# Optimization experiments

Hardware: AMD Instinct MI355X
Metric: run time of the kernel (lower is better)

Reference implementation:

```python
import jax, jax.numpy as jnp
import numpy as np

B, T, D = 64, 512, 1024  # batch, step_dim, feature_dim


def setup_inputs() -> dict:
    key = jax.random.key(0)
    k1, k2, k3, k4, k5 = jax.random.split(key, 5)
    x = jax.random.normal(k1, (B, T, D), dtype=jnp.float32)
    mask = jax.random.randint(k2, (B, T), 0, 2).astype(bool)
    mask = mask.at[:, 0].set(True)  # guarantee >=1 valid token per row
    # xavier_uniform bounds
    w_bound = float(np.sqrt(6.0 / (D + D)))
    c_bound = float(np.sqrt(6.0 / (T + 1)))
    weight = jax.random.uniform(k3, (D, D), minval=-w_bound, maxval=w_bound, dtype=jnp.float32)
    context_vector = jax.random.uniform(k4, (T, 1), minval=-c_bound, maxval=c_bound, dtype=jnp.float32)
    b = jnp.zeros((T,), dtype=jnp.float32)
    return {"x": x, "mask": mask, "weight": weight, "context_vector": context_vector, "b": b}


def reference(x, mask, weight, context_vector, b):
    # batched bilinear scores: eij[b,t,s] = x[b,t,:] @ W @ x[b,s,:]^T
    xw = jnp.einsum('btd,de->bte', x, weight)          # [B,T,D]
    eij = jnp.einsum('bte,bse->bts', xw, x)            # [B,T,T]
    # bias over last axis (matches view(-1, T) + b), tanh
    eij = jnp.tanh(eij + b)                            # [B,T,T]
    # context-vector reduction over last axis -> [B,T]
    scores = jnp.einsum('bts,s->bt', eij, context_vector[:, 0])
    # masked softmax over T
    scores = jnp.where(mask, scores, -jnp.inf)
    a = jax.nn.softmax(scores, axis=1)                 # [B,T]
    # weighted sum of inputs -> [B,D]
    out = jnp.einsum('btd,bt->bd', x, a)
    return (out, a)
```

## Files before the change

kernel.cpp:

```cpp
#include <hip/hip_runtime.h>
#include <hip/hip_bf16.h>
#include <math.h>

#define B_ 64
#define T_ 512
#define D_ 1024
#define M_ (B_*T_)

typedef unsigned short u16;
typedef __attribute__((ext_vector_type(8))) _Float16 f16x8;
typedef __attribute__((ext_vector_type(4))) float f32x4;

__device__ __forceinline__ u16 f2h(float f) {
  union { _Float16 h; u16 u; } v;
  v.h = (_Float16)f;
  return v.u;
}

__device__ __forceinline__ float h2f(u16 u) {
  union { u16 u; _Float16 h; } v;
  v.u = u;
  return (float)v.h;
}

__device__ __forceinline__ float fast_tanh(float x) {
  return 1.0f - 2.0f / (__expf(2.0f * x) + 1.0f);
}

__device__ __forceinline__ void gll16(const void* g, void* l) {
  __builtin_amdgcn_global_load_lds(
      (const __attribute__((address_space(1))) unsigned int*)g,
      (__attribute__((address_space(3))) unsigned int*)l, 16, 0, 0);
}

__global__ __launch_bounds__(256) void cvt_x_kernel(const float4* __restrict__ x,
                                                    ushort4* __restrict__ xh, int n4) {
  int i = blockIdx.x * 256 + threadIdx.x;
  if (i < n4) {
    float4 v = x[i];
    ushort4 o;
    o.x = f2h(v.x); o.y = f2h(v.y); o.z = f2h(v.z); o.w = f2h(v.w);
    xh[i] = o;
  }
}

__global__ __launch_bounds__(1024) void cvt_wt_kernel(const float* __restrict__ W,
                                                      u16* __restrict__ Wt) {
  __shared__ float tile[32][33];
  int tx = threadIdx.x & 31, ty = threadIdx.x >> 5;
  int n0 = blockIdx.x * 32, k0 = blockIdx.y * 32;
  tile[ty][tx] = W[(k0 + ty) * D_ + n0 + tx];
  __syncthreads();
  Wt[(n0 + ty) * D_ + k0 + tx] = f2h(tile[tx][ty]);
}


__device__ __forceinline__ void gemm_core128(const u16* __restrict__ Abase,
                                             const u16* __restrict__ Bbase, int K,
                                             u16* As, u16* Bs, int tid, f32x4 acc[4][4]) {
  const int wave = tid >> 6, lane = tid & 63;
  const int swz_c = ((lane & 3) - ((lane >> 3) & 3)) & 3;
  const int rin = lane >> 2;
  const u16* gA[2]; u16* lA[2];
  const u16* gB[2]; u16* lB[2];
#pragma unroll
  for (int j = 0; j < 2; j++) {
    int ci = wave * 2 + j;
    gA[j] = Abase + (long)(ci * 16 + rin) * K + swz_c * 8;
    lA[j] = As + ci * 512;
    gB[j] = Bbase + (long)(ci * 16 + rin) * K + swz_c * 8;
    lB[j] = Bs + ci * 512;
  }
  const int wrow = (wave >> 1) * 64, wcol = (wave & 1) * 64;
  const int lm = lane & 15, qd = lane >> 4;
  const int swz_r = ((qd + (lm >> 1)) & 3) * 8;
  const u16* ra = As + (wrow + lm) * 32 + swz_r;
  const u16* rb = Bs + (wcol + lm) * 32 + swz_r;

  for (int kt = 0; kt < K; kt += 32) {
#pragma unroll
    for (int j = 0; j < 2; j++) {
      gll16(gA[j], lA[j]); gA[j] += 32;
      gll16(gB[j], lB[j]); gB[j] += 32;
    }
    __syncthreads();
    f16x8 af[4], bfr[4];
#pragma unroll
    for (int i = 0; i < 4; i++) {
      af[i] = *(const f16x8*)(ra + i * 512);
      bfr[i] = *(const f16x8*)(rb + i * 512);
    }
#pragma unroll
    for (int mi = 0; mi < 4; mi++)
#pragma unroll
      for (int ni = 0; ni < 4; ni++)
        acc[mi][ni] = __builtin_amdgcn_mfma_f32_16x16x32_f16(af[mi], bfr[ni], acc[mi][ni], 0, 0, 0);
    __syncthreads();
  }
}

__global__ __launch_bounds__(256, 4) void gemm1_kernel(const u16* __restrict__ xh,
                                                       const u16* __restrict__ wt,
                                                       u16* __restrict__ xw) {
  __shared__ u16 As[128 * 32], Bs[128 * 32];
  f32x4 acc[4][4] = {};
  const int tid = threadIdx.x;
  const int bx = blockIdx.x;
  const int xcd = bx & 7, j = bx >> 3;
  const int mt = xcd * 32 + (j >> 3);
  const int nt = j & 7;
  const long m0 = (long)mt * 128;
  const long n0 = (long)nt * 128;
  gemm_core128(xh + m0 * D_, wt + n0 * D_, D_, As, Bs, tid, acc);

  const int wave = tid >> 6, lane = tid & 63;
  const int wrow = (wave >> 1) * 64, wcol = (wave & 1) * 64;
  const int lm = lane & 15, qd = lane >> 4;
#pragma unroll
  for (int mi = 0; mi < 4; mi++)
#pragma unroll
    for (int ni = 0; ni < 4; ni++) {
      long m = m0 + wrow + mi * 16 + qd * 4;
      long n = n0 + wcol + ni * 16 + lm;
      u16* p = xw + m * D_ + n;
#pragma unroll
      for (int r = 0; r < 4; r++) p[(long)r * D_] = f2h(acc[mi][ni][r]);
    }
}

__global__ __launch_bounds__(256, 4) void gemm2_kernel(const u16* __restrict__ xw,
                                                       const u16* __restrict__ xh,
                                                       const float* __restrict__ bias,
                                                       const float* __restrict__ cv,
                                                       float* __restrict__ scores_part) {
  __shared__ u16 As[128 * 32], Bs[128 * 32];
  f32x4 acc[4][4] = {};
  const int bx = blockIdx.x;
  const int xcd = bx & 7, j = bx >> 3;
  const int bb = xcd * 8 + (j >> 4);
  const int tile = j & 15;
  const int tt = tile >> 2, st = tile & 3;
  const int tid = threadIdx.x;
  const long arow = (long)bb * T_ + tt * 128;
  const long brow = (long)bb * T_ + st * 128;
  gemm_core128(xw + arow * D_, xh + brow * D_, D_, As, Bs, tid, acc);

  const int wave = tid >> 6, lane = tid & 63;
  const int wrow = (wave >> 1) * 64, wcol = (wave & 1) * 64;
  const int lm = lane & 15, qd = lane >> 4;
  float cvv[4], bv[4];
#pragma unroll
  for (int ni = 0; ni < 4; ni++) {
    int s = st * 128 + wcol + ni * 16 + lm;
    cvv[ni] = cv[s];
    bv[ni] = bias[s];
  }
  const int plane = st * 2 + (wave & 1);
  float* dst = scores_part + plane * (B_ * T_) + bb * T_ + tt * 128;
#pragma unroll
  for (int mi = 0; mi < 4; mi++) {
#pragma unroll
    for (int r = 0; r < 4; r++) {
      float p = 0.f;
#pragma unroll
      for (int ni = 0; ni < 4; ni++) p += fast_tanh(acc[mi][ni][r] + bv[ni]) * cvv[ni];
      p += __shfl_xor(p, 1); p += __shfl_xor(p, 2);
      p += __shfl_xor(p, 4); p += __shfl_xor(p, 8);
      if (lm == 0) dst[wrow + mi * 16 + qd * 4 + r] = p;
    }
  }
}

__global__ __launch_bounds__(512) void softmax_kernel(const float* __restrict__ sp,
                                                      const unsigned char* __restrict__ m8,
                                                      float* __restrict__ a_out) {
  const int b = blockIdx.x, t = threadIdx.x;
  __shared__ int nonz;
  __shared__ float redm[8], reds[8];
  if (t == 0) nonz = 0;
  __syncthreads();
  unsigned char c = m8[t * 4 + 1] | m8[t * 4 + 2] | m8[t * 4 + 3];
  if (c) atomicOr(&nonz, 1);
  __syncthreads();
  const bool is_i32 = (nonz == 0);
  const int idx = b * T_ + t;
  const bool valid = is_i32 ? (m8[(long)idx * 4] != 0) : (m8[idx] != 0);

  float val = 0.f;
#pragma unroll
  for (int pl = 0; pl < 8; pl++) val += sp[pl * (B_ * T_) + idx];
  if (!valid) val = -INFINITY;
  float m = val;
#pragma unroll
  for (int o = 32; o > 0; o >>= 1) m = fmaxf(m, __shfl_xor(m, o));
  const int wv = t >> 6, ln = t & 63;
  if (ln == 0) redm[wv] = m;
  __syncthreads();
  float rowmax = redm[0];
#pragma unroll
  for (int i = 1; i < 8; i++) rowmax = fmaxf(rowmax, redm[i]);

  float e = valid ? expf(val - rowmax) : 0.f;
  float ssum = e;
#pragma unroll
  for (int o = 32; o > 0; o >>= 1) ssum += __shfl_xor(ssum, o);
  if (ln == 0) reds[wv] = ssum;
  __syncthreads();
  float tot = 0.f;
#pragma unroll
  for (int i = 0; i < 8; i++) tot += reds[i];
  a_out[idx] = e / tot;
}

__global__ __launch_bounds__(256) void wsum_kernel(const u16* __restrict__ xh,
                                                   const float* __restrict__ a,
                                                   float* __restrict__ out) {
  __shared__ float4 lred[4][64];
  const int b = blockIdx.x, dq = blockIdx.y, tid = threadIdx.x;
  const int w = tid >> 6, lane = tid & 63;
  const int d0 = dq * 256 + lane * 4;
  const u16* xp = xh + (long)b * T_ * D_ + d0;
  const float* ap = a + b * T_;
  float4 acc = make_float4(0.f, 0.f, 0.f, 0.f);
  for (int i = 0; i < 128; i++) {
    int t = w * 128 + i;
    float av = ap[t];
    ushort4 xv = *(const ushort4*)(xp + (long)t * D_);
    acc.x += av * h2f(xv.x); acc.y += av * h2f(xv.y);
    acc.z += av * h2f(xv.z); acc.w += av * h2f(xv.w);
  }
  lred[w][lane] = acc;
  __syncthreads();
  if (w == 0) {
    float4 s0 = lred[0][lane], s1 = lred[1][lane], s2 = lred[2][lane], s3 = lred[3][lane];
    float4 s;
    s.x = s0.x + s1.x + s2.x + s3.x;
    s.y = s0.y + s1.y + s2.y + s3.y;
    s.z = s0.z + s1.z + s2.z + s3.z;
    s.w = s0.w + s1.w + s2.w + s3.w;
    *(float4*)(out + (long)b * D_ + d0) = s;
  }
}

extern "C" void kernel_launch(void* const* d_in, const int* in_sizes, int n_in,
                              void* d_out, int out_size, void* d_ws, size_t ws_size,
                              hipStream_t stream) {
  const float* x = (const float*)d_in[0];
  const unsigned char* mask = (const unsigned char*)d_in[1];
  const float* W = (const float*)d_in[2];
  const float* cv = (const float*)d_in[3];
  const float* bias = (const float*)d_in[4];

  float* out = (float*)d_out;
  float* a_out = out + (size_t)B_ * D_;

  char* ws = (char*)d_ws;
  u16* xh = (u16*)(ws);
  u16* wt = (u16*)(ws + 67108864);
  float* scores_part = (float*)(ws + 67108864);
  u16* xw = (u16*)(ws + 69206016);

  cvt_x_kernel<<<(M_ * D_ / 4 + 255) / 256, 256, 0, stream>>>((const float4*)x,
                                                              (ushort4*)xh, M_ * D_ / 4);
  cvt_wt_kernel<<<dim3(32, 32), 1024, 0, stream>>>(W, wt);
  gemm1_kernel<<<2048, 256, 0, stream>>>(xh, wt, xw);
  gemm2_kernel<<<1024, 256, 0, stream>>>(xw, xh, bias, cv, scores_part);
  softmax_kernel<<<B_, 512, 0, stream>>>(scores_part, mask, a_out);
  wsum_kernel<<<dim3(B_, 4), 256, 0, stream>>>(xh, a_out, out);
}
```

Baseline: 344.4 us.

## Enlarge gemm1 tiles, merge conversion kernels, fuse softmax with weighted sum

gemm1 becomes a standalone kernel with a 256x128 output tile and a K-step of 64. It uses a new XOR-style LDS swizzle and drops to 2 blocks per CU, aiming for more data reuse per load and fewer barriers. The x and W conversion kernels are merged into a single launch, and the softmax and weighted-sum kernels are fused. Each fused block recomputes the softmax for its batch row, removing a launch and a global round-trip for the attention weights. The costs are higher register and LDS pressure in gemm1 and softmax work repeated four times per batch row.

```diff
diff --git a/kernel.cpp b/kernel.cpp
--- a/kernel.cpp
+++ b/kernel.cpp
@@ -33,27 +33,112 @@
       (__attribute__((address_space(3))) unsigned int*)l, 16, 0, 0);
 }
 
-__global__ __launch_bounds__(256) void cvt_x_kernel(const float4* __restrict__ x,
-                                                    ushort4* __restrict__ xh, int n4) {
-  int i = blockIdx.x * 256 + threadIdx.x;
-  if (i < n4) {
+__global__ __launch_bounds__(256) void cvt_kernel(const float4* __restrict__ x,
+                                                  ushort4* __restrict__ xh,
+                                                  const float* __restrict__ W,
+                                                  u16* __restrict__ wt) {
+  __shared__ float tile[32][33];
+  const int bid = blockIdx.x;
+  if (bid < 32768) {
+    int i = bid * 256 + threadIdx.x;
     float4 v = x[i];
     ushort4 o;
     o.x = f2h(v.x); o.y = f2h(v.y); o.z = f2h(v.z); o.w = f2h(v.w);
     xh[i] = o;
-  }
-}
-
-__global__ __launch_bounds__(1024) void cvt_wt_kernel(const float* __restrict__ W,
-                                                      u16* __restrict__ Wt) {
-  __shared__ float tile[32][33];
-  int tx = threadIdx.x & 31, ty = threadIdx.x >> 5;
-  int n0 = blockIdx.x * 32, k0 = blockIdx.y * 32;
-  tile[ty][tx] = W[(k0 + ty) * D_ + n0 + tx];
-  __syncthreads();
-  Wt[(n0 + ty) * D_ + k0 + tx] = f2h(tile[tx][ty]);
-}
-
+  } else {
+    const int tb = bid - 32768;
+    const int n0 = (tb & 31) * 32, k0 = (tb >> 5) * 32;
+    const int tx = threadIdx.x & 31, ty = threadIdx.x >> 5;
+#pragma unroll
+    for (int ph = 0; ph < 4; ph++)
+      tile[ty + ph * 8][tx] = W[(k0 + ty + ph * 8) * D_ + n0 + tx];
+    __syncthreads();
+#pragma unroll
+    for (int ph = 0; ph < 4; ph++)
+      wt[(long)(n0 + ty + ph * 8) * D_ + k0 + tx] = f2h(tile[tx][ty + ph * 8]);
+  }
+}
+
+__global__ __launch_bounds__(256, 2) void gemm1_kernel(const u16* __restrict__ xh,
+                                                       const u16* __restrict__ wt,
+                                                       u16* __restrict__ xw) {
+  __shared__ u16 As[256 * 64];
+  __shared__ u16 Bs[128 * 64];
+  f32x4 acc[8][4] = {};
+  const int tid = threadIdx.x;
+  const int bx = blockIdx.x;
+  const int xcd = bx & 7, j = bx >> 3;
+  const int mt = xcd * 16 + (j >> 3);
+  const int nt = j & 7;
+  const long m0 = (long)mt * 256;
+  const long n0 = (long)nt * 128;
+  const u16* Abase = xh + m0 * D_;
+  const u16* Bbase = wt + n0 * D_;
+
+  const int wave = tid >> 6, lane = tid & 63;
+  const int p = lane & 7, rl = lane >> 3;
+
+  const u16* gA[8]; u16* lA[8];
+#pragma unroll
+  for (int i = 0; i < 8; i++) {
+    int g = wave * 8 + i;
+    int r = g * 8 + rl;
+    int c = (p - (r >> 1)) & 7;
+    gA[i] = Abase + (long)r * D_ + c * 8;
+    lA[i] = As + g * 512;
+  }
+  const u16* gB[4]; u16* lB[4];
+#pragma unroll
+  for (int i = 0; i < 4; i++) {
+    int g = wave * 4 + i;
+    int r = g * 8 + rl;
+    int c = (p - (r >> 1)) & 7;
+    gB[i] = Bbase + (long)r * D_ + c * 8;
+    lB[i] = Bs + g * 512;
+  }
+
+  const int wrow = (wave >> 1) * 128, wcol = (wave & 1) * 64;
+  const int lm = lane & 15, qd = lane >> 4;
+  const u16* ra = As + (wrow + lm) * 64;
+  const u16* rb = Bs + (wcol + lm) * 64;
+  const int pk0 = ((qd + (lm >> 1)) & 7) * 8;
+  const int pk1 = ((qd + 4 + (lm >> 1)) & 7) * 8;
+
+  for (int kt = 0; kt < D_; kt += 64) {
+#pragma unroll
+    for (int i = 0; i < 8; i++) { gll16(gA[i], lA[i]); gA[i] += 64; }
+#pragma unroll
+    for (int i = 0; i < 4; i++) { gll16(gB[i], lB[i]); gB[i] += 64; }
+    __syncthreads();
+#pragma unroll
+    for (int kk = 0; kk < 2; kk++) {
+      const int pk = kk ? pk1 : pk0;
+      f16x8 af[8], bfr[4];
+#pragma unroll
+      for (int i = 0; i < 8; i++) af[i] = *(const f16x8*)(ra + i * 16 * 64 + pk);
+#pragma unroll
+      for (int i = 0; i < 4; i++) bfr[i] = *(const f16x8*)(rb + i * 16 * 64 + pk);
+#pragma unroll
+      for (int mi = 0; mi < 8; mi++)
+#pragma unroll
+        for (int ni = 0; ni < 4; ni++)
+          acc[mi][ni] = __builtin_amdgcn_mfma_f32_16x16x32_f16(af[mi], bfr[ni], acc[mi][ni], 0, 0, 0);
+    }
+    __syncthreads();
+  }
+
+  const int lm2 = lane & 15, qd2 = lane >> 4;
+#pragma unroll
+  for (int mi = 0; mi < 8; mi++)
+#pragma unroll
+    for (int ni = 0; ni < 4; ni++) {
+      long m = m0 + wrow + mi * 16 + qd2 * 4;
+      long n = n0 + wcol + ni * 16 + lm2;
+      u16* ptr = xw + m * D_ + n;
+#pragma unroll
+      for (int r = 0; r < 4; r++) ptr[(long)r * D_] = f2h(acc[mi][ni][r]);
+    }
+}
 
 __device__ __forceinline__ void gemm_core128(const u16* __restrict__ Abase,
                                              const u16* __restrict__ Bbase, int K,
@@ -97,35 +182,6 @@
         acc[mi][ni] = __builtin_amdgcn_mfma_f32_16x16x32_f16(af[mi], bfr[ni], acc[mi][ni], 0, 0, 0);
     __syncthreads();
   }
-}
-
-__global__ __launch_bounds__(256, 4) void gemm1_kernel(const u16* __restrict__ xh,
-                                                       const u16* __restrict__ wt,
-                                                       u16* __restrict__ xw) {
-  __shared__ u16 As[128 * 32], Bs[128 * 32];
-  f32x4 acc[4][4] = {};
-  const int tid = threadIdx.x;
-  const int bx = blockIdx.x;
-  const int xcd = bx & 7, j = bx >> 3;
-  const int mt = xcd * 32 + (j >> 3);
-  const int nt = j & 7;
-  const long m0 = (long)mt * 128;
-  const long n0 = (long)nt * 128;
-  gemm_core128(xh + m0 * D_, wt + n0 * D_, D_, As, Bs, tid, acc);
-
-  const int wave = tid >> 6, lane = tid & 63;
-  const int wrow = (wave >> 1) * 64, wcol = (wave & 1) * 64;
-  const int lm = lane & 15, qd = lane >> 4;
-#pragma unroll
-  for (int mi = 0; mi < 4; mi++)
-#pragma unroll
-    for (int ni = 0; ni < 4; ni++) {
-      long m = m0 + wrow + mi * 16 + qd * 4;
-      long n = n0 + wcol + ni * 16 + lm;
-      u16* p = xw + m * D_ + n;
-#pragma unroll
-      for (int r = 0; r < 4; r++) p[(long)r * D_] = f2h(acc[mi][ni][r]);
-    }
 }
 
 __global__ __launch_bounds__(256, 4) void gemm2_kernel(const u16* __restrict__ xw,
@@ -171,68 +227,72 @@
   }
 }
 
-__global__ __launch_bounds__(512) void softmax_kernel(const float* __restrict__ sp,
+__global__ __launch_bounds__(256) void sm_wsum_kernel(const float* __restrict__ sp,
                                                       const unsigned char* __restrict__ m8,
-                                                      float* __restrict__ a_out) {
-  const int b = blockIdx.x, t = threadIdx.x;
+                                                      const u16* __restrict__ xh,
+                                                      float* __restrict__ a_out,
+                                                      float* __restrict__ out) {
+  __shared__ float a_sh[512];
+  __shared__ float red[8];
   __shared__ int nonz;
-  __shared__ float redm[8], reds[8];
-  if (t == 0) nonz = 0;
-  __syncthreads();
-  unsigned char c = m8[t * 4 + 1] | m8[t * 4 + 2] | m8[t * 4 + 3];
-  if (c) atomicOr(&nonz, 1);
-  __syncthreads();
-  const bool is_i32 = (nonz == 0);
-  const int idx = b * T_ + t;
-  const bool valid = is_i32 ? (m8[(long)idx * 4] != 0) : (m8[idx] != 0);
-
-  float val = 0.f;
-#pragma unroll
-  for (int pl = 0; pl < 8; pl++) val += sp[pl * (B_ * T_) + idx];
-  if (!valid) val = -INFINITY;
-  float m = val;
-#pragma unroll
-  for (int o = 32; o > 0; o >>= 1) m = fmaxf(m, __shfl_xor(m, o));
-  const int wv = t >> 6, ln = t & 63;
-  if (ln == 0) redm[wv] = m;
-  __syncthreads();
-  float rowmax = redm[0];
-#pragma unroll
-  for (int i = 1; i < 8; i++) rowmax = fmaxf(rowmax, redm[i]);
-
-  float e = valid ? expf(val - rowmax) : 0.f;
-  float ssum = e;
-#pragma unroll
-  for (int o = 32; o > 0; o >>= 1) ssum += __shfl_xor(ssum, o);
-  if (ln == 0) reds[wv] = ssum;
-  __syncthreads();
-  float tot = 0.f;
-#pragma unroll
-  for (int i = 0; i < 8; i++) tot += reds[i];
-  a_out[idx] = e / tot;
-}
-
-__global__ __launch_bounds__(256) void wsum_kernel(const u16* __restrict__ xh,
-                                                   const float* __restrict__ a,
-                                                   float* __restrict__ out) {
   __shared__ float4 lred[4][64];
   const int b = blockIdx.x, dq = blockIdx.y, tid = threadIdx.x;
-  const int w = tid >> 6, lane = tid & 63;
-  const int d0 = dq * 256 + lane * 4;
+  const int w = tid >> 6, ln = tid & 63;
+  if (tid == 0) nonz = 0;
+  __syncthreads();
+  {
+    unsigned char c = m8[tid * 4 + 1] | m8[tid * 4 + 2] | m8[tid * 4 + 3] |
+                      m8[(tid + 256) * 4 + 1] | m8[(tid + 256) * 4 + 2] | m8[(tid + 256) * 4 + 3];
+    if (c) atomicOr(&nonz, 1);
+  }
+  __syncthreads();
+  const bool is_i32 = (nonz == 0);
+  float v[2]; bool valid[2];
+#pragma unroll
+  for (int h = 0; h < 2; h++) {
+    int t = tid + h * 256;
+    int idx = b * T_ + t;
+    valid[h] = is_i32 ? (m8[(long)idx * 4] != 0) : (m8[idx] != 0);
+    float s = 0.f;
+#pragma unroll
+    for (int pl = 0; pl < 8; pl++) s += sp[pl * (B_ * T_) + idx];
+    v[h] = valid[h] ? s : -INFINITY;
+  }
+  float m = fmaxf(v[0], v[1]);
+#pragma unroll
+  for (int o = 32; o > 0; o >>= 1) m = fmaxf(m, __shfl_xor(m, o));
+  if (ln == 0) red[w] = m;
+  __syncthreads();
+  const float rowmax = fmaxf(fmaxf(red[0], red[1]), fmaxf(red[2], red[3]));
+  float e0 = valid[0] ? expf(v[0] - rowmax) : 0.f;
+  float e1 = valid[1] ? expf(v[1] - rowmax) : 0.f;
+  float ss = e0 + e1;
+#pragma unroll
+  for (int o = 32; o > 0; o >>= 1) ss += __shfl_xor(ss, o);
+  if (ln == 0) red[4 + w] = ss;
+  __syncthreads();
+  const float tot = red[4] + red[5] + red[6] + red[7];
+  const float a0 = e0 / tot, a1 = e1 / tot;
+  a_sh[tid] = a0; a_sh[tid + 256] = a1;
+  if (dq == 0) {
+    a_out[b * T_ + tid] = a0;
+    a_out[b * T_ + tid + 256] = a1;
+  }
+  __syncthreads();
+  const int d0 = dq * 256 + ln * 4;
   const u16* xp = xh + (long)b * T_ * D_ + d0;
-  const float* ap = a + b * T_;
   float4 acc = make_float4(0.f, 0.f, 0.f, 0.f);
   for (int i = 0; i < 128; i++) {
     int t = w * 128 + i;
-    float av = ap[t];
+    float av = a_sh[t];
     ushort4 xv = *(const ushort4*)(xp + (long)t * D_);
     acc.x += av * h2f(xv.x); acc.y += av * h2f(xv.y);
     acc.z += av * h2f(xv.z); acc.w += av * h2f(xv.w);
   }
-  lred[w][lane] = acc;
+  lred[w][ln] = acc;
   __syncthreads();
   if (w == 0) {
-    float4 s0 = lred[0][lane], s1 = lred[1][lane], s2 = lred[2][lane], s3 = lred[3][lane];
+    float4 s0 = lred[0][ln], s1 = lred[1][ln], s2 = lred[2][ln], s3 = lred[3][ln];
     float4 s;
     s.x = s0.x + s1.x + s2.x + s3.x;
     s.y = s0.y + s1.y + s2.y + s3.y;
@@ -260,11 +320,8 @@
   float* scores_part = (float*)(ws + 67108864);
   u16* xw = (u16*)(ws + 69206016);
 
-  cvt_x_kernel<<<(M_ * D_ / 4 + 255) / 256, 256, 0, stream>>>((const float4*)x,
-                                                              (ushort4*)xh, M_ * D_ / 4);
-  cvt_wt_kernel<<<dim3(32, 32), 1024, 0, stream>>>(W, wt);
-  gemm1_kernel<<<2048, 256, 0, stream>>>(xh, wt, xw);
+  cvt_kernel<<<32768 + 1024, 256, 0, stream>>>((const float4*)x, (ushort4*)xh, W, wt);
+  gemm1_kernel<<<1024, 256, 0, stream>>>(xh, wt, xw);
   gemm2_kernel<<<1024, 256, 0, stream>>>(xw, xh, bias, cv, scores_part);
-  softmax_kernel<<<B_, 512, 0, stream>>>(scores_part, mask, a_out);
-  wsum_kernel<<<dim3(B_, 4), 256, 0, stream>>>(xh, a_out, out);
-}
+  sm_wsum_kernel<<<dim3(B_, 4), 256, 0, stream>>>(scores_part, mask, xh, a_out, out);
+}
```

After: 323.4 us. 6.1% less time.
